# Kernel optimization log

Measured on AMD Instinct MI355X. Metric: run time of the kernel, lower is better.

## Reference

```python
import jax, jax.numpy as jnp
import numpy as np

MARGIN = 1.0


def setup_inputs() -> dict:
    key = jax.random.key(0)
    k1, k2, k3 = jax.random.split(key, 3)
    n, d = 8192, 128
    feat1 = jax.random.normal(k1, (n, d), dtype=jnp.float32)
    feat2 = jax.random.normal(k2, (n, d), dtype=jnp.float32)
    # similarity labels in {+1, -1}, as expected by HingeEmbeddingLoss
    simi = (2 * jax.random.randint(k3, (n, n), 0, 2) - 1).astype(jnp.int32)
    return {"feat1": feat1, "feat2": feat2, "simi": simi}


def reference(feat1, feat2, simi):
    # logits[i,j] = -||feat1_i - feat2_j||^2, computed without the O(n*m*d) expand
    sq1 = jnp.sum(feat1 * feat1, axis=-1, keepdims=True)          # [n, 1]
    sq2 = jnp.sum(feat2 * feat2, axis=-1)                          # [m]
    cross = jnp.einsum('nd,md->nm', feat1, feat2)                  # [n, m]
    logits = -(sq1 + sq2[None, :] - 2.0 * cross)                   # [n, m]
    probs = jax.nn.softmax(logits, axis=1)                         # [n, m]
    # HingeEmbeddingLoss: x if y==1 else max(0, margin - x); mean reduction
    loss = jnp.where(simi == 1, probs, jnp.maximum(0.0, MARGIN - probs))
    return jnp.mean(loss)
```

## Files before the change

### kernel.cpp

```cpp
#include <hip/hip_runtime.h>
#include <hip/hip_bf16.h>
#include <stdint.h>

#define N 8192
#define D 128
#define NCHUNK 16
#define CHUNK (N / NCHUNK)
#define RT 64
#define CT 64
#define NTILES (CHUNK / CT)
#define NBLK (N / RT * NCHUNK)

typedef short bf16x8 __attribute__((ext_vector_type(8)));
typedef float f32x4 __attribute__((ext_vector_type(4)));
typedef unsigned int uint32;

#define OFF_ACC   0u
#define OFF_SQ2   1024u
#define OFF_BCNT  (OFF_SQ2 + N * 4u)
#define OFF_M     (OFF_BCNT + NBLK * 4u)
#define OFF_L     (OFF_M + NCHUNK * N * 4u)
#define OFF_S     (OFF_L + NCHUNK * N * 4u)
#define OFF_F1    (OFF_S + NCHUNK * N * 4u)
#define OFF_F2    (OFF_F1 + N * D * 2u)

#define GLLDS16(gp, lp)                                                        \
    __builtin_amdgcn_global_load_lds(                                          \
        (const __attribute__((address_space(1))) uint32*)(gp),                 \
        (__attribute__((address_space(3))) uint32*)(lp), 16, 0, 0)

__global__ __launch_bounds__(256)
void prep_kernel(const float* __restrict__ f1, const float* __restrict__ f2,
                 unsigned short* __restrict__ f1b, unsigned short* __restrict__ f2b,
                 float* __restrict__ sq2) {
    const int w    = blockIdx.x * 4 + (threadIdx.x >> 6);
    const int lane = threadIdx.x & 63;
    for (int row = w; row < N; row += 1024) {
        float a0 = f1[row * D + lane];
        float a1 = f1[row * D + 64 + lane];
        float b0 = f2[row * D + lane];
        float b1 = f2[row * D + 64 + lane];
        __hip_bfloat16 t;
        t = __float2bfloat16(a0); f1b[row * D + lane]      = *(unsigned short*)&t;
        t = __float2bfloat16(a1); f1b[row * D + 64 + lane] = *(unsigned short*)&t;
        t = __float2bfloat16(b0); f2b[row * D + lane]      = *(unsigned short*)&t;
        t = __float2bfloat16(b1); f2b[row * D + 64 + lane] = *(unsigned short*)&t;
        float ss = b0 * b0 + b1 * b1;
        #pragma unroll
        for (int off = 32; off > 0; off >>= 1) ss += __shfl_xor(ss, off);
        if (lane == 0) sq2[row] = ss;
    }
}

__global__ __launch_bounds__(256)
void main_kernel(const unsigned short* __restrict__ f1b,
                 const unsigned short* __restrict__ f2b,
                 const float* __restrict__ sq2,
                 const int* __restrict__ simi,
                 float* __restrict__ pm, float* __restrict__ pl, float* __restrict__ ps,
                 uint32* __restrict__ blockcnt) {
    __shared__ unsigned short ldsB[CT * D];
    __shared__ uint32 maskMem[2 * 4 * 4 * 256];
    __shared__ uint32 cred[4];

    const int tid  = threadIdx.x;
    const int wave = tid >> 6;
    const int lane = tid & 63;
    const int lo   = lane & 15;
    const int hi   = lane >> 4;

    const int rowtile = blockIdx.x;
    const int chunk   = blockIdx.y;
    const int rbase   = rowtile * RT + wave * 16;
    const int cbase0  = chunk * CHUNK;

    bf16x8 afrag[4];
    {
        const unsigned short* ap = f1b + (size_t)(rbase + lo) * D + hi * 8;
        #pragma unroll
        for (int kk = 0; kk < 4; kk++)
            afrag[kk] = *reinterpret_cast<const bf16x8*>(ap + kk * 32);
    }

    const int sq_ = (tid >> 4);
    const int sg_ = tid & 15;
    const unsigned short* stg_p[4];
    unsigned short* lds_p[4];
    #pragma unroll
    for (int it = 0; it < 4; it++) {
        int q = it * 16 + sq_;
        int c = 4 * (q & 15) + (q >> 4);
        stg_p[it] = f2b + (size_t)(cbase0 + c) * D + sg_ * 8;
        lds_p[it] = ldsB + q * D + ((sg_ ^ (q & 15)) * 8);
    }

    const int* simi_p = simi + (size_t)(rbase + hi * 4) * N + cbase0 + 4 * lo;
    const float* sqv_p = sq2 + cbase0 + 4 * lo;
    uint32* mbase[2];
    mbase[0] = maskMem + wave * 4 * 256;
    mbase[1] = maskMem + (4 + wave) * 4 * 256;

    float m[4], l[4], s[4];
    #pragma unroll
    for (int r = 0; r < 4; r++) { m[r] = -1e30f; l[r] = 0.f; s[r] = 0.f; }
    uint32 cnt = 0;

    #pragma unroll
    for (int r = 0; r < 4; r++)
        GLLDS16(simi_p + (size_t)r * N, mbase[0] + r * 256);
    uint4 vstg[4];
    #pragma unroll
    for (int it = 0; it < 4; it++)
        vstg[it] = *reinterpret_cast<const uint4*>(stg_p[it]);
    f32x4 sqv = *reinterpret_cast<const f32x4*>(sqv_p);

    for (int t = 0; t < NTILES; t++) {
        __syncthreads();
        #pragma unroll
        for (int it = 0; it < 4; it++)
            *reinterpret_cast<uint4*>(lds_p[it]) = vstg[it];
        __syncthreads();

        const uint32* mk = mbase[t & 1];
        uint32 mb[4];
        #pragma unroll
        for (int r = 0; r < 4; r++) {
            int4 v = *reinterpret_cast<const int4*>(mk + r * 256 + lane * 4);
            uint32 nib = (uint32)(v.x == 1) | ((uint32)(v.y == 1) << 1) |
                         ((uint32)(v.z == 1) << 2) | ((uint32)(v.w == 1) << 3);
            mb[r] = nib;
            cnt += 4u - __popc(nib);
        }
        f32x4 sqv_t = sqv;

        if (t + 1 < NTILES) {
            const int* sp = simi_p + CT;
            #pragma unroll
            for (int r = 0; r < 4; r++)
                GLLDS16(sp + (size_t)r * N, mbase[(t + 1) & 1] + r * 256);
            #pragma unroll
            for (int it = 0; it < 4; it++)
                vstg[it] = *reinterpret_cast<const uint4*>(stg_p[it] + (size_t)(t + 1) * CT * D);
            sqv = *reinterpret_cast<const f32x4*>(sqv_p + (t + 1) * CT);
            simi_p = sp;
        }

        f32x4 acc[4];
        #pragma unroll
        for (int cf = 0; cf < 4; cf++) {
            acc[cf] = (f32x4){0.f, 0.f, 0.f, 0.f};
            const int brow = cf * 16 + lo;
            #pragma unroll
            for (int kk = 0; kk < 4; kk++) {
                int g = kk * 4 + hi;
                bf16x8 b = *reinterpret_cast<const bf16x8*>(
                    ldsB + brow * D + ((g ^ (brow & 15)) * 8));
                acc[cf] = __builtin_amdgcn_mfma_f32_16x16x32_bf16(afrag[kk], b, acc[cf], 0, 0, 0);
            }
        }

        #pragma unroll
        for (int r = 0; r < 4; r++) {
            float lg[4];
            #pragma unroll
            for (int cf = 0; cf < 4; cf++)
                lg[cf] = 2.0f * acc[cf][r] - sqv_t[cf];
            float tm = fmaxf(fmaxf(lg[0], lg[1]), fmaxf(lg[2], lg[3]));
            float mn = fmaxf(m[r], tm);
            float al = __expf(m[r] - mn);
            m[r] = mn;
            float p[4];
            #pragma unroll
            for (int cf = 0; cf < 4; cf++) p[cf] = __expf(lg[cf] - mn);
            l[r] = l[r] * al + ((p[0] + p[1]) + (p[2] + p[3]));
            float sm = 0.f;
            #pragma unroll
            for (int cf = 0; cf < 4; cf++)
                sm += ((mb[r] >> cf) & 1u) ? p[cf] : 0.f;
            s[r] = s[r] * al + sm;
        }
    }

    #pragma unroll
    for (int r = 0; r < 4; r++) {
        float M = m[r];
        #pragma unroll
        for (int off = 1; off < 16; off <<= 1)
            M = fmaxf(M, __shfl_xor(M, off));
        float sc = __expf(m[r] - M);
        float L = l[r] * sc, S = s[r] * sc;
        #pragma unroll
        for (int off = 1; off < 16; off <<= 1) {
            L += __shfl_xor(L, off);
            S += __shfl_xor(S, off);
        }
        if (lo == 0) {
            int row = rbase + hi * 4 + r;
            int idx = chunk * N + row;
            pm[idx] = M; pl[idx] = L; ps[idx] = S;
        }
    }

    #pragma unroll
    for (int off = 1; off < 64; off <<= 1) cnt += __shfl_xor(cnt, off);
    if (lane == 0) cred[wave] = cnt;
    __syncthreads();
    if (tid == 0)
        blockcnt[blockIdx.y * 128 + blockIdx.x] = cred[0] + cred[1] + cred[2] + cred[3];
}

__global__ void merge_kernel(const float* __restrict__ pm, const float* __restrict__ pl,
                             const float* __restrict__ ps, const uint32* __restrict__ blockcnt,
                             float* __restrict__ s_acc, uint32* __restrict__ neg_acc) {
    const int row = blockIdx.x * 256 + threadIdx.x;
    float M = -1e30f;
    #pragma unroll
    for (int k = 0; k < NCHUNK; k++) M = fmaxf(M, pm[k * N + row]);
    float L = 0.f, S = 0.f;
    #pragma unroll
    for (int k = 0; k < NCHUNK; k++) {
        float e = __expf(pm[k * N + row] - M);
        L += pl[k * N + row] * e;
        S += ps[k * N + row] * e;
    }
    float r = S / L;
    uint32 pc = (threadIdx.x < 64) ? blockcnt[blockIdx.x * 64 + threadIdx.x] : 0u;
    #pragma unroll
    for (int off = 32; off > 0; off >>= 1) {
        r  += __shfl_xor(r, off);
        pc += __shfl_xor(pc, off);
    }
    __shared__ float red[4];
    __shared__ uint32 redp[4];
    int lane = threadIdx.x & 63, w = threadIdx.x >> 6;
    if (lane == 0) { red[w] = r; redp[w] = pc; }
    __syncthreads();
    if (threadIdx.x == 0) {
        atomicAdd(s_acc, red[0] + red[1] + red[2] + red[3]);
        atomicAdd(neg_acc, redp[0] + redp[1] + redp[2] + redp[3]);
    }
}

__global__ void final_kernel(const float* __restrict__ s_acc, const uint32* __restrict__ neg_acc,
                             float* __restrict__ out) {
    double S = (double)s_acc[0];
    double C = (double)neg_acc[0];
    double n = (double)N;
    out[0] = (float)((2.0 * S + C - n) / (n * n));
}

extern "C" void kernel_launch(void* const* d_in, const int* in_sizes, int n_in,
                              void* d_out, int out_size, void* d_ws, size_t ws_size,
                              hipStream_t stream) {
    const float* f1   = (const float*)d_in[0];
    const float* f2   = (const float*)d_in[1];
    const int*   simi = (const int*)d_in[2];
    float* out = (float*)d_out;
    char* ws = (char*)d_ws;

    float*  acc_s    = (float*)(ws + OFF_ACC);
    uint32* acc_n    = (uint32*)(ws + OFF_ACC + 4);
    float*  sq2      = (float*)(ws + OFF_SQ2);
    uint32* blockcnt = (uint32*)(ws + OFF_BCNT);
    float*  pm       = (float*)(ws + OFF_M);
    float*  pl       = (float*)(ws + OFF_L);
    float*  ps       = (float*)(ws + OFF_S);
    unsigned short* f1b = (unsigned short*)(ws + OFF_F1);
    unsigned short* f2b = (unsigned short*)(ws + OFF_F2);

    hipMemsetAsync(ws + OFF_ACC, 0, 64, stream);
    prep_kernel<<<256, 256, 0, stream>>>(f1, f2, f1b, f2b, sq2);
    main_kernel<<<dim3(N / RT, NCHUNK), 256, 0, stream>>>(f1b, f2b, sq2, simi,
                                                          pm, pl, ps, blockcnt);
    merge_kernel<<<N / 256, 256, 0, stream>>>(pm, pl, ps, blockcnt, acc_s, acc_n);
    final_kernel<<<1, 1, 0, stream>>>(acc_s, acc_n, out);
}
```

Baseline: 426.2 us.

## Pre-permute feat2 into MFMA fragment layout and drop LDS staging

Adds a prep kernel that writes feat2 as bf16 in MFMA B-fragment order so the main kernel loads B operands directly from global memory, removing LDS staging and both per-tile block barriers. The simi mask is prefetched into registers instead of via global_load_lds, and the column split is halved to 8 chunks. This removes synchronisation but each wave now fetches B independently, raising L2 traffic and lowering block count.

```diff
diff --git a/kernel.cpp b/kernel.cpp
--- a/kernel.cpp
+++ b/kernel.cpp
@@ -4,7 +4,7 @@
 
 #define N 8192
 #define D 128
-#define NCHUNK 16
+#define NCHUNK 8
 #define CHUNK (N / NCHUNK)
 #define RT 64
 #define CT 64
@@ -22,17 +22,11 @@
 #define OFF_L     (OFF_M + NCHUNK * N * 4u)
 #define OFF_S     (OFF_L + NCHUNK * N * 4u)
 #define OFF_F1    (OFF_S + NCHUNK * N * 4u)
-#define OFF_F2    (OFF_F1 + N * D * 2u)
-
-#define GLLDS16(gp, lp)                                                        \
-    __builtin_amdgcn_global_load_lds(                                          \
-        (const __attribute__((address_space(1))) uint32*)(gp),                 \
-        (__attribute__((address_space(3))) uint32*)(lp), 16, 0, 0)
+#define OFF_F2T   (OFF_F1 + N * D * 2u)
 
 __global__ __launch_bounds__(256)
 void prep_kernel(const float* __restrict__ f1, const float* __restrict__ f2,
-                 unsigned short* __restrict__ f1b, unsigned short* __restrict__ f2b,
-                 float* __restrict__ sq2) {
+                 unsigned short* __restrict__ f1b, float* __restrict__ sq2) {
     const int w    = blockIdx.x * 4 + (threadIdx.x >> 6);
     const int lane = threadIdx.x & 63;
     for (int row = w; row < N; row += 1024) {
@@ -43,8 +37,6 @@
         __hip_bfloat16 t;
         t = __float2bfloat16(a0); f1b[row * D + lane]      = *(unsigned short*)&t;
         t = __float2bfloat16(a1); f1b[row * D + 64 + lane] = *(unsigned short*)&t;
-        t = __float2bfloat16(b0); f2b[row * D + lane]      = *(unsigned short*)&t;
-        t = __float2bfloat16(b1); f2b[row * D + 64 + lane] = *(unsigned short*)&t;
         float ss = b0 * b0 + b1 * b1;
         #pragma unroll
         for (int off = 32; off > 0; off >>= 1) ss += __shfl_xor(ss, off);
@@ -53,14 +45,34 @@
 }
 
 __global__ __launch_bounds__(256)
+void prep2_kernel(const float* __restrict__ f2, unsigned short* __restrict__ f2T) {
+    const int t64  = blockIdx.x;
+    const int cf   = threadIdx.x >> 6;
+    const int lane = threadIdx.x & 63;
+    const int lo   = lane & 15;
+    const int hi   = lane >> 4;
+    const int col  = t64 * 64 + 4 * lo + cf;
+    #pragma unroll
+    for (int kk = 0; kk < 4; kk++) {
+        const float* src = f2 + (size_t)col * D + (kk * 4 + hi) * 8;
+        bf16x8 o;
+        #pragma unroll
+        for (int j = 0; j < 8; j++) {
+            __hip_bfloat16 t = __float2bfloat16(src[j]);
+            o[j] = *reinterpret_cast<short*>(&t);
+        }
+        *reinterpret_cast<bf16x8*>(
+            f2T + ((size_t)t64 * 16 + cf * 4 + kk) * 512 + lane * 8) = o;
+    }
+}
+
+__global__ __launch_bounds__(256)
 void main_kernel(const unsigned short* __restrict__ f1b,
-                 const unsigned short* __restrict__ f2b,
+                 const unsigned short* __restrict__ f2T,
                  const float* __restrict__ sq2,
                  const int* __restrict__ simi,
                  float* __restrict__ pm, float* __restrict__ pl, float* __restrict__ ps,
                  uint32* __restrict__ blockcnt) {
-    __shared__ unsigned short ldsB[CT * D];
-    __shared__ uint32 maskMem[2 * 4 * 4 * 256];
     __shared__ uint32 cred[4];
 
     const int tid  = threadIdx.x;
@@ -69,10 +81,10 @@
     const int lo   = lane & 15;
     const int hi   = lane >> 4;
 
-    const int rowtile = blockIdx.x;
-    const int chunk   = blockIdx.y;
-    const int rbase   = rowtile * RT + wave * 16;
-    const int cbase0  = chunk * CHUNK;
+    const int rbase  = blockIdx.x * RT + wave * 16;
+    const int chunk  = blockIdx.y;
+    const int cbase0 = chunk * CHUNK;
+    const int T0     = chunk * NTILES;
 
     bf16x8 afrag[4];
     {
@@ -82,50 +94,26 @@
             afrag[kk] = *reinterpret_cast<const bf16x8*>(ap + kk * 32);
     }
 
-    const int sq_ = (tid >> 4);
-    const int sg_ = tid & 15;
-    const unsigned short* stg_p[4];
-    unsigned short* lds_p[4];
-    #pragma unroll
-    for (int it = 0; it < 4; it++) {
-        int q = it * 16 + sq_;
-        int c = 4 * (q & 15) + (q >> 4);
-        stg_p[it] = f2b + (size_t)(cbase0 + c) * D + sg_ * 8;
-        lds_p[it] = ldsB + q * D + ((sg_ ^ (q & 15)) * 8);
-    }
-
-    const int* simi_p = simi + (size_t)(rbase + hi * 4) * N + cbase0 + 4 * lo;
+    const int* simi_p  = simi + (size_t)(rbase + hi * 4) * N + cbase0 + 4 * lo;
     const float* sqv_p = sq2 + cbase0 + 4 * lo;
-    uint32* mbase[2];
-    mbase[0] = maskMem + wave * 4 * 256;
-    mbase[1] = maskMem + (4 + wave) * 4 * 256;
+    const unsigned short* bT = f2T + (size_t)T0 * 8192 + lane * 8;
 
     float m[4], l[4], s[4];
     #pragma unroll
     for (int r = 0; r < 4; r++) { m[r] = -1e30f; l[r] = 0.f; s[r] = 0.f; }
     uint32 cnt = 0;
 
+    int4 mkv[4];
     #pragma unroll
     for (int r = 0; r < 4; r++)
-        GLLDS16(simi_p + (size_t)r * N, mbase[0] + r * 256);
-    uint4 vstg[4];
-    #pragma unroll
-    for (int it = 0; it < 4; it++)
-        vstg[it] = *reinterpret_cast<const uint4*>(stg_p[it]);
+        mkv[r] = *reinterpret_cast<const int4*>(simi_p + (size_t)r * N);
     f32x4 sqv = *reinterpret_cast<const f32x4*>(sqv_p);
 
     for (int t = 0; t < NTILES; t++) {
-        __syncthreads();
-        #pragma unroll
-        for (int it = 0; it < 4; it++)
-            *reinterpret_cast<uint4*>(lds_p[it]) = vstg[it];
-        __syncthreads();
-
-        const uint32* mk = mbase[t & 1];
         uint32 mb[4];
         #pragma unroll
         for (int r = 0; r < 4; r++) {
-            int4 v = *reinterpret_cast<const int4*>(mk + r * 256 + lane * 4);
+            int4 v = mkv[r];
             uint32 nib = (uint32)(v.x == 1) | ((uint32)(v.y == 1) << 1) |
                          ((uint32)(v.z == 1) << 2) | ((uint32)(v.w == 1) << 3);
             mb[r] = nib;
@@ -134,27 +122,21 @@
         f32x4 sqv_t = sqv;
 
         if (t + 1 < NTILES) {
-            const int* sp = simi_p + CT;
+            simi_p += CT;
             #pragma unroll
             for (int r = 0; r < 4; r++)
-                GLLDS16(sp + (size_t)r * N, mbase[(t + 1) & 1] + r * 256);
-            #pragma unroll
-            for (int it = 0; it < 4; it++)
-                vstg[it] = *reinterpret_cast<const uint4*>(stg_p[it] + (size_t)(t + 1) * CT * D);
+                mkv[r] = *reinterpret_cast<const int4*>(simi_p + (size_t)r * N);
             sqv = *reinterpret_cast<const f32x4*>(sqv_p + (t + 1) * CT);
-            simi_p = sp;
         }
 
         f32x4 acc[4];
         #pragma unroll
         for (int cf = 0; cf < 4; cf++) {
             acc[cf] = (f32x4){0.f, 0.f, 0.f, 0.f};
-            const int brow = cf * 16 + lo;
+            const unsigned short* bp = bT + ((size_t)t * 16 + cf * 4) * 512;
             #pragma unroll
             for (int kk = 0; kk < 4; kk++) {
-                int g = kk * 4 + hi;
-                bf16x8 b = *reinterpret_cast<const bf16x8*>(
-                    ldsB + brow * D + ((g ^ (brow & 15)) * 8));
+                bf16x8 b = *reinterpret_cast<const bf16x8*>(bp + kk * 512);
                 acc[cf] = __builtin_amdgcn_mfma_f32_16x16x32_bf16(afrag[kk], b, acc[cf], 0, 0, 0);
             }
         }
@@ -224,7 +206,7 @@
         S += ps[k * N + row] * e;
     }
     float r = S / L;
-    uint32 pc = (threadIdx.x < 64) ? blockcnt[blockIdx.x * 64 + threadIdx.x] : 0u;
+    uint32 pc = (threadIdx.x < 32) ? blockcnt[blockIdx.x * 32 + threadIdx.x] : 0u;
     #pragma unroll
     for (int off = 32; off > 0; off >>= 1) {
         r  += __shfl_xor(r, off);
@@ -266,11 +248,12 @@
     float*  pl       = (float*)(ws + OFF_L);
     float*  ps       = (float*)(ws + OFF_S);
     unsigned short* f1b = (unsigned short*)(ws + OFF_F1);
-    unsigned short* f2b = (unsigned short*)(ws + OFF_F2);
+    unsigned short* f2T = (unsigned short*)(ws + OFF_F2T);
 
     hipMemsetAsync(ws + OFF_ACC, 0, 64, stream);
-    prep_kernel<<<256, 256, 0, stream>>>(f1, f2, f1b, f2b, sq2);
-    main_kernel<<<dim3(N / RT, NCHUNK), 256, 0, stream>>>(f1b, f2b, sq2, simi,
+    prep_kernel<<<256, 256, 0, stream>>>(f1, f2, f1b, sq2);
+    prep2_kernel<<<N / 64, 256, 0, stream>>>(f2, f2T);
+    main_kernel<<<dim3(N / RT, NCHUNK), 256, 0, stream>>>(f1b, f2T, sq2, simi,
                                                           pm, pl, ps, blockcnt);
     merge_kernel<<<N / 256, 256, 0, stream>>>(pm, pl, ps, blockcnt, acc_s, acc_n);
     final_kernel<<<1, 1, 0, stream>>>(acc_s, acc_n, out);
```

New measurement: 419.6 us. No clear change (-1.5%).
